# Optimization experiments

Hardware: AMD Instinct MI355X
Metric: run time of the kernel (lower is better)

The kernel has to match this reference:

```python
import jax, jax.numpy as jnp
import numpy as np

N, B, E, H = 16384, 16, 131072, 2
NPG = N // B  # nodes per graph
DIMS = [128, 256, 512]  # in==out channels per GAT layer


def setup_inputs() -> dict:
    key = jax.random.key(0)
    ks = iter(jax.random.split(key, 40))
    inp = {"node_feats": jax.random.normal(next(ks), (N, DIMS[0]), jnp.float32)}
    for l, d in enumerate(DIMS):
        s = 1.0 / np.sqrt(d)
        inp[f"W{l}"] = jax.random.normal(next(ks), (d, H * d), jnp.float32) * s
        inp[f"attnl{l}"] = jax.random.normal(next(ks), (H, d), jnp.float32) * 0.1
        inp[f"attnr{l}"] = jax.random.normal(next(ks), (H, d), jnp.float32) * 0.1
        inp[f"resW{l}"] = jax.random.normal(next(ks), (d, H * d), jnp.float32) * s
        inp[f"gamma{l}"] = jnp.ones((d,), jnp.float32)
        inp[f"beta{l}"] = jnp.zeros((d,), jnp.float32)
        inp[f"alpha{l}"] = jnp.ones((d,), jnp.float32)
    dst = jax.random.randint(next(ks), (E,), 0, N, jnp.int32)
    # source node sampled from the same graph as the destination
    src = (dst // NPG) * NPG + jax.random.randint(next(ks), (E,), 0, NPG, jnp.int32)
    inp["edge_src"] = src
    inp["edge_dst"] = dst
    inp["graph_ids"] = jnp.repeat(jnp.arange(B, dtype=jnp.int32), NPG)
    return inp


def _gat(x, W, al, ar, rW, src, dst, d):
    # x: [N, in]; W,rW: [in, H*d]; al,ar: [H,d]
    h = (x @ W).reshape(N, H, d)
    el = jnp.sum(h * al, -1)  # [N,H]
    er = jnp.sum(h * ar, -1)  # [N,H]
    e = jax.nn.leaky_relu(el[src] + er[dst], 0.2)  # [E,H]
    m = jax.ops.segment_max(e, dst, num_segments=N)
    ex = jnp.exp(e - m[dst])
    a = ex / jax.ops.segment_sum(ex, dst, num_segments=N)[dst]  # edge softmax
    out = jax.ops.segment_sum(h[src] * a[:, :, None], dst, num_segments=N)
    return out + (x @ rW).reshape(N, H, d)  # residual projection


def _gnorm(x, gamma, beta, alpha, eps=1e-5):
    # GraphNorm: (x - alpha*mean) / std * gamma + beta, stats over all nodes/heads
    mean = jnp.mean(x, axis=(0, 1), keepdims=True)
    sh = x - alpha * mean
    var = jnp.mean(sh * sh, axis=(0, 1), keepdims=True)
    return gamma * sh * jax.lax.rsqrt(var + eps) + beta


def reference(node_feats, W0, attnl0, attnr0, resW0, gamma0, beta0, alpha0,
              W1, attnl1, attnr1, resW1, gamma1, beta1, alpha1,
              W2, attnl2, attnr2, resW2, gamma2, beta2, alpha2,
              edge_src, edge_dst, graph_ids):
    params = [(W0, attnl0, attnr0, resW0, gamma0, beta0, alpha0),
              (W1, attnl1, attnr1, resW1, gamma1, beta1, alpha1),
              (W2, attnl2, attnr2, resW2, gamma2, beta2, alpha2)]
    counts = jax.ops.segment_sum(jnp.ones((N,), jnp.float32), graph_ids, num_segments=B)
    x = node_feats
    parts = []
    for l, d in enumerate(DIMS):
        W, al, ar, rW, g, b, a_ = params[l]
        x = _gat(x.reshape(N, -1), W, al, ar, rW, edge_src, edge_dst, d)  # [N,H,d]
        x = _gnorm(x, g, b, a_)
        x = jax.nn.leaky_relu(x, 0.01)
        nm = x.mean(1)  # [N,d] head-mean stored as 'updated_feats'
        parts.append(jax.ops.segment_sum(nm, graph_ids, num_segments=B) / counts[:, None])
    return jax.nn.leaky_relu(jnp.concatenate(parts, -1), 0.01)  # [B, 896]
```

## Files before the change

### kernel.cpp

```cpp
#include <hip/hip_runtime.h>
#include <math.h>

constexpr int NNODES  = 16384;
constexpr int NEDGES  = 131072;
constexpr int NGRAPHS = 16;

typedef short bf16x8 __attribute__((ext_vector_type(8)));
typedef short bf16x4 __attribute__((ext_vector_type(4)));
typedef float f32x4  __attribute__((ext_vector_type(4)));

__device__ __forceinline__ float leaky(float x, float s){ return x >= 0.0f ? x : s * x; }

__device__ __forceinline__ unsigned short f2bf(float f){
  unsigned u = __builtin_bit_cast(unsigned, f);
  u += 0x7FFFu + ((u >> 16) & 1u);
  return (unsigned short)(u >> 16);
}
__device__ __forceinline__ float bf2f(unsigned short u){
  unsigned x = (unsigned)u << 16; return __builtin_bit_cast(float, x);
}

__device__ __forceinline__ void gload_lds16(const unsigned short* g, unsigned short* l){
  __builtin_amdgcn_global_load_lds((const __attribute__((address_space(1))) void*)g,
                                   (__attribute__((address_space(3))) void*)l, 16, 0, 0);
}

__global__ void k_deg(const int* __restrict__ dst, int* __restrict__ deg){
  int e = blockIdx.x * 256 + threadIdx.x;
  if (e < NEDGES) atomicAdd(&deg[dst[e]], 1);
}

__global__ __launch_bounds__(1024) void k_scan(const int* __restrict__ deg,
                                               int* __restrict__ rowptr,
                                               int* __restrict__ cursor){
  __shared__ int sums[1024];
  int t = threadIdx.x;
  int loc[16];
  int s = 0;
  #pragma unroll
  for (int i = 0; i < 16; i++){ loc[i] = deg[t*16 + i]; s += loc[i]; }
  sums[t] = s; __syncthreads();
  for (int off = 1; off < 1024; off <<= 1){
    int v = (t >= off) ? sums[t - off] : 0;
    __syncthreads();
    sums[t] += v;
    __syncthreads();
  }
  int base = (t > 0) ? sums[t-1] : 0;
  #pragma unroll
  for (int i = 0; i < 16; i++){
    rowptr[t*16 + i] = base; cursor[t*16 + i] = base; base += loc[i];
  }
  if (t == 1023) rowptr[NNODES] = base;
}

__global__ void k_scatter(const int* __restrict__ src, const int* __restrict__ dst,
                          int* __restrict__ cursor, int* __restrict__ perm){
  int e = blockIdx.x * 256 + threadIdx.x;
  if (e < NEDGES){ int p = atomicAdd(&cursor[dst[e]], 1); perm[p] = src[e]; }
}

__global__ __launch_bounds__(256) void k_counts(const int* __restrict__ gid, float* __restrict__ counts){
  __shared__ int h[NGRAPHS];
  int t = threadIdx.x;
  if (t < NGRAPHS) h[t] = 0;
  __syncthreads();
  int base = blockIdx.x * 1024;
  #pragma unroll
  for (int i = 0; i < 4; i++)
    atomicAdd(&h[gid[base + t + i*256]], 1);
  __syncthreads();
  if (t < NGRAPHS && h[t] > 0) atomicAdd(&counts[t], (float)h[t]);
}

__global__ void k_cvt(const float* __restrict__ in, unsigned short* __restrict__ out, int n4){
  int i = blockIdx.x * 256 + threadIdx.x;
  if (i >= n4) return;
  float4 v = ((const float4*)in)[i];
  ushort4 o; o.x = f2bf(v.x); o.y = f2bf(v.y); o.z = f2bf(v.z); o.w = f2bf(v.w);
  ((ushort4*)out)[i] = o;
}

__global__ __launch_bounds__(256) void k_cvt_t2(const float* __restrict__ W,
                                                const float* __restrict__ RW,
                                                unsigned short* __restrict__ Wt,
                                                unsigned short* __restrict__ RWt,
                                                int K, int NN){
  __shared__ float tile[32][33];
  const float* src = blockIdx.z ? RW : W;
  unsigned short* dst = blockIdx.z ? RWt : Wt;
  int n0 = blockIdx.x * 32, k0 = blockIdx.y * 32;
  int tx = threadIdx.x & 31, ty = threadIdx.x >> 5;
  #pragma unroll
  for (int i = 0; i < 4; i++)
    tile[ty + i*8][tx] = src[(size_t)(k0 + ty + i*8) * NN + n0 + tx];
  __syncthreads();
  #pragma unroll
  for (int i = 0; i < 4; i++)
    dst[(size_t)(n0 + ty + i*8) * K + k0 + tx] = f2bf(tile[tx][ty + i*8]);
}

__global__ __launch_bounds__(256) void k_gemm2(const unsigned short* __restrict__ A,
                                               const unsigned short* __restrict__ Wt,
                                               const unsigned short* __restrict__ RWt,
                                               unsigned short* __restrict__ HB,
                                               unsigned short* __restrict__ RB,
                                               const float* __restrict__ al,
                                               const float* __restrict__ ar,
                                               float* __restrict__ elp,
                                               float* __restrict__ erp,
                                               int K, int NN){
  __shared__ unsigned short As[2][128 * 64];
  __shared__ unsigned short Bs[2][128 * 64];
  int t = threadIdx.x;
  int lane = t & 63, w = t >> 6;
  int nx  = gridDim.x;
  int nwg = nx * gridDim.y;
  int bid = blockIdx.x + blockIdx.y * nx;
  int wg  = (bid & 7) * (nwg >> 3) + (bid >> 3);
  int bx = wg % nx, by = wg / nx;
  int half = nx >> 1;
  bool isW = bx < half;
  const unsigned short* Bt = isW ? Wt : RWt;
  int colB = (isW ? bx : bx - half) * 128;
  int rowA = by * 128;

  int wr = (w >> 1) * 64, wc = (w & 1) * 64;
  int l16 = lane & 15, lhi = lane >> 4;
  int r8  = lane >> 3;
  int kcs = (((lane & 7) * 16) ^ (r8 << 4)) >> 1;
  f32x4 acc[4][4] = {};

  const unsigned short* Ap = A  + (size_t)(rowA) * K + kcs;
  const unsigned short* Bp = Bt + (size_t)(colB) * K + kcs;

  int nt = K >> 6;
  #pragma unroll
  for (int i = 0; i < 4; i++){
    int c = w * 4 + i;
    int row = c * 8 + r8;
    gload_lds16(Ap + (size_t)row * K, &As[0][c * 512]);
    gload_lds16(Bp + (size_t)row * K, &Bs[0][c * 512]);
  }
  __syncthreads();

  int cur = 0;
  for (int tI = 0; tI < nt; tI++){
    if (tI + 1 < nt){
      int k0n = (tI + 1) << 6;
      #pragma unroll
      for (int i = 0; i < 4; i++){
        int c = w * 4 + i;
        int row = c * 8 + r8;
        gload_lds16(Ap + (size_t)row * K + k0n, &As[cur ^ 1][c * 512]);
        gload_lds16(Bp + (size_t)row * K + k0n, &Bs[cur ^ 1][c * 512]);
      }
    }
    bf16x8 af[4][2], bfr[4][2];
    #pragma unroll
    for (int mi = 0; mi < 4; mi++){
      int row = wr + mi * 16 + l16;
      #pragma unroll
      for (int s = 0; s < 2; s++){
        int k = s * 32 + lhi * 8;
        int off = row * 128 + ((k * 2) ^ ((row & 7) << 4));
        af[mi][s] = *(const bf16x8*)((const char*)As[cur] + off);
      }
    }
    #pragma unroll
    for (int ni = 0; ni < 4; ni++){
      int row = wc + ni * 16 + l16;
      #pragma unroll
      for (int s = 0; s < 2; s++){
        int k = s * 32 + lhi * 8;
        int off = row * 128 + ((k * 2) ^ ((row & 7) << 4));
        bfr[ni][s] = *(const bf16x8*)((const char*)Bs[cur] + off);
      }
    }
    #pragma unroll
    for (int mi = 0; mi < 4; mi++)
      #pragma unroll
      for (int ni = 0; ni < 4; ni++){
        acc[mi][ni] = __builtin_amdgcn_mfma_f32_16x16x32_bf16(af[mi][0], bfr[ni][0], acc[mi][ni], 0, 0, 0);
        acc[mi][ni] = __builtin_amdgcn_mfma_f32_16x16x32_bf16(af[mi][1], bfr[ni][1], acc[mi][ni], 0, 0, 0);
      }
    __syncthreads();
    cur ^= 1;
  }

  unsigned short* C = isW ? HB : RB;
  #pragma unroll
  for (int mi = 0; mi < 4; mi++){
    #pragma unroll
    for (int j = 0; j < 4; j++){
      int r = rowA + wr + mi * 16 + lhi * 4 + j;
      unsigned short* Cp = C + (size_t)r * NN + colB + wc + l16;
      #pragma unroll
      for (int ni = 0; ni < 4; ni++)
        Cp[ni * 16] = f2bf(acc[mi][ni][j]);
    }
  }

  if (isW){
    int G = NN >> 6;
    int g64 = (colB + wc) >> 6;
    float alv[4], arv[4];
    #pragma unroll
    for (int ni = 0; ni < 4; ni++){
      int col = colB + wc + ni * 16 + l16;
      alv[ni] = al[col]; arv[ni] = ar[col];
    }
    #pragma unroll
    for (int mi = 0; mi < 4; mi++){
      #pragma unroll
      for (int j = 0; j < 4; j++){
        float pe = acc[mi][0][j]*alv[0] + acc[mi][1][j]*alv[1]
                 + acc[mi][2][j]*alv[2] + acc[mi][3][j]*alv[3];
        float pr = acc[mi][0][j]*arv[0] + acc[mi][1][j]*arv[1]
                 + acc[mi][2][j]*arv[2] + acc[mi][3][j]*arv[3];
        #pragma unroll
        for (int o = 8; o; o >>= 1){ pe += __shfl_xor(pe, o); pr += __shfl_xor(pr, o); }
        if (l16 == 0){
          int r = rowA + wr + mi * 16 + lhi * 4 + j;
          elp[(size_t)r * G + g64] = pe;
          erp[(size_t)r * G + g64] = pr;
        }
      }
    }
  }
}

__global__ void k_elred(const float* __restrict__ elp, const float* __restrict__ erp,
                        float* __restrict__ el, float* __restrict__ er, int G){
  int row = blockIdx.x * 256 + threadIdx.x;
  int half = G >> 1;
  float s0 = 0.f, s1 = 0.f, q0 = 0.f, q1 = 0.f;
  const float* ep = elp + (size_t)row * G;
  const float* rp = erp + (size_t)row * G;
  for (int i = 0; i < half; i++){ s0 += ep[i]; q0 += rp[i]; }
  for (int i = half; i < G; i++){ s1 += ep[i]; q1 += rp[i]; }
  el[row*2] = s0; el[row*2+1] = s1;
  er[row*2] = q0; er[row*2+1] = q1;
}

template<int D>
__global__ __launch_bounds__(256) void k_attn(const unsigned short* __restrict__ HB,
                                              unsigned short* __restrict__ RB,
                                              const float* __restrict__ el,
                                              const float* __restrict__ er,
                                              const int* __restrict__ rowptr,
                                              const int* __restrict__ perm){
  constexpr int ITER = (2*D)/256;
  int wid = threadIdx.x >> 6, lane = threadIdx.x & 63;
  int nb = (blockIdx.x & 7) * (NNODES/4/8) + (blockIdx.x >> 3);
  int n = nb * 4 + wid;
  int r0 = rowptr[n], r1 = rowptr[n+1];
  if (r0 == r1) return;
  float er0 = er[n*2], er1 = er[n*2+1];
  float mx0 = -1e30f, mx1 = -1e30f;
  for (int e = r0 + lane; e < r1; e += 64){
    int s = perm[e];
    mx0 = fmaxf(mx0, leaky(el[s*2]   + er0, 0.2f));
    mx1 = fmaxf(mx1, leaky(el[s*2+1] + er1, 0.2f));
  }
  #pragma unroll
  for (int o = 32; o; o >>= 1){ mx0 = fmaxf(mx0, __shfl_xor(mx0, o)); mx1 = fmaxf(mx1, __shfl_xor(mx1, o)); }
  float sm0 = 0.0f, sm1 = 0.0f;
  for (int e = r0 + lane; e < r1; e += 64){
    int s = perm[e];
    sm0 += expf(leaky(el[s*2]   + er0, 0.2f) - mx0);
    sm1 += expf(leaky(el[s*2+1] + er1, 0.2f) - mx1);
  }
  #pragma unroll
  for (int o = 32; o; o >>= 1){ sm0 += __shfl_xor(sm0, o); sm1 += __shfl_xor(sm1, o); }
  float inv0 = 1.0f / sm0, inv1 = 1.0f / sm1;
  float acc[ITER][4];
  #pragma unroll
  for (int j = 0; j < ITER; j++)
    #pragma unroll
    for (int i = 0; i < 4; i++) acc[j][i] = 0.0f;
  for (int e = r0; e < r1; ++e){
    int s = perm[e];
    float a0 = expf(leaky(el[s*2]   + er0, 0.2f) - mx0) * inv0;
    float a1 = expf(leaky(el[s*2+1] + er1, 0.2f) - mx1) * inv1;
    const unsigned short* hrow = HB + (size_t)s * (2*D);
    #pragma unroll
    for (int j = 0; j < ITER; j++){
      int base = j*256 + lane*4;
      bf16x4 v = *(const bf16x4*)(hrow + base);
      float a = (base < D) ? a0 : a1;
      #pragma unroll
      for (int i = 0; i < 4; i++)
        acc[j][i] += a * bf2f((unsigned short)v[i]);
    }
  }
  unsigned short* rrow = RB + (size_t)n * (2*D);
  #pragma unroll
  for (int j = 0; j < ITER; j++){
    int base = j*256 + lane*4;
    bf16x4 r = *(bf16x4*)(rrow + base);
    ushort4 o;
    o.x = f2bf(bf2f((unsigned short)r[0]) + acc[j][0]);
    o.y = f2bf(bf2f((unsigned short)r[1]) + acc[j][1]);
    o.z = f2bf(bf2f((unsigned short)r[2]) + acc[j][2]);
    o.w = f2bf(bf2f((unsigned short)r[3]) + acc[j][3]);
    *(ushort4*)(rrow + base) = o;
  }
}

__global__ __launch_bounds__(256) void k_stats(const unsigned short* __restrict__ R, int nn,
                                               float* __restrict__ gsum, float* __restrict__ gsq){
  int t = threadIdx.x, lane = t & 63, w = t >> 6;
  int c = blockIdx.y * 256 + lane * 4;
  const unsigned short* base = R + (size_t)(blockIdx.x * 128 + w) * nn + c;
  float4 s = make_float4(0,0,0,0), q = make_float4(0,0,0,0);
  #pragma unroll 4
  for (int i = 0; i < 32; i++){
    bf16x4 bv = *(const bf16x4*)(base + (size_t)(i * 4) * nn);
    float vx = bf2f((unsigned short)bv[0]), vy = bf2f((unsigned short)bv[1]);
    float vz = bf2f((unsigned short)bv[2]), vw = bf2f((unsigned short)bv[3]);
    s.x += vx; s.y += vy; s.z += vz; s.w += vw;
    q.x += vx*vx; q.y += vy*vy; q.z += vz*vz; q.w += vw*vw;
  }
  __shared__ float4 rs[256], rq[256];
  rs[t] = s; rq[t] = q; __syncthreads();
  if (t < 64){
    float4 a = rs[t], b = rs[t+64], c2 = rs[t+128], d2 = rs[t+192];
    float4 e = rq[t], f = rq[t+64], g2 = rq[t+128], h2 = rq[t+192];
    int cc = blockIdx.y * 256 + t * 4;
    atomicAdd(&gsum[cc+0], a.x+b.x+c2.x+d2.x);
    atomicAdd(&gsum[cc+1], a.y+b.y+c2.y+d2.y);
    atomicAdd(&gsum[cc+2], a.z+b.z+c2.z+d2.z);
    atomicAdd(&gsum[cc+3], a.w+b.w+c2.w+d2.w);
    atomicAdd(&gsq [cc+0], e.x+f.x+g2.x+h2.x);
    atomicAdd(&gsq [cc+1], e.y+f.y+g2.y+h2.y);
    atomicAdd(&gsq [cc+2], e.z+f.z+g2.z+h2.z);
    atomicAdd(&gsq [cc+3], e.w+f.w+g2.w+h2.w);
  }
}

__global__ __launch_bounds__(256) void k_norm_pool(const unsigned short* __restrict__ R,
                                                   unsigned short* __restrict__ Xn,
                                                   const float* __restrict__ gsum,
                                                   const float* __restrict__ gsq,
                                                   const float* __restrict__ gamma,
                                                   const float* __restrict__ beta,
                                                   const float* __restrict__ alpha,
                                                   float* __restrict__ pool, int d, int loff){
  int t = threadIdx.x, lane = t & 63, w = t >> 6;
  int c = blockIdx.y * 256 + lane * 4;
  int cm = c & (d - 1);
  int nodeb = blockIdx.x * 128;
  int g = blockIdx.x >> 3;
  int nn = 2 * d;
  const float Minv = 1.0f / (2.0f * (float)NNODES);
  float4 gg = *(const float4*)(gamma + cm);
  float4 bb = *(const float4*)(beta + cm);
  float4 aa = *(const float4*)(alpha + cm);
  float mmv[4], rrv[4];
  #pragma unroll
  for (int i = 0; i < 4; i++){
    float m = (gsum[cm+i] + gsum[cm+i+d]) * Minv;
    float q = (gsq [cm+i] + gsq [cm+i+d]) * Minv;
    float a = (i==0)?aa.x:(i==1)?aa.y:(i==2)?aa.z:aa.w;
    float var = q - a * m * m * (2.0f - a);
    mmv[i] = m; rrv[i] = rsqrtf(var + 1e-5f);
  }
  float am0 = aa.x*mmv[0], am1 = aa.y*mmv[1], am2 = aa.z*mmv[2], am3 = aa.w*mmv[3];
  const unsigned short* base = R + (size_t)(nodeb + w) * nn + c;
  unsigned short* xb = Xn ? (Xn + (size_t)(nodeb + w) * nn + c) : nullptr;
  float4 accp = make_float4(0,0,0,0);
  #pragma unroll 4
  for (int i = 0; i < 32; i++){
    bf16x4 bv = *(const bf16x4*)(base + (size_t)(i * 4) * nn);
    float vx = bf2f((unsigned short)bv[0]), vy = bf2f((unsigned short)bv[1]);
    float vz = bf2f((unsigned short)bv[2]), vw = bf2f((unsigned short)bv[3]);
    float y0 = gg.x*(vx-am0)*rrv[0] + bb.x; y0 = y0 >= 0.f ? y0 : 0.01f*y0;
    float y1 = gg.y*(vy-am1)*rrv[1] + bb.y; y1 = y1 >= 0.f ? y1 : 0.01f*y1;
    float y2 = gg.z*(vz-am2)*rrv[2] + bb.z; y2 = y2 >= 0.f ? y2 : 0.01f*y2;
    float y3 = gg.w*(vw-am3)*rrv[3] + bb.w; y3 = y3 >= 0.f ? y3 : 0.01f*y3;
    if (xb){
      ushort4 o; o.x = f2bf(y0); o.y = f2bf(y1); o.z = f2bf(y2); o.w = f2bf(y3);
      *(ushort4*)(xb + (size_t)(i * 4) * nn) = o;
    }
    accp.x += y0; accp.y += y1; accp.z += y2; accp.w += y3;
  }
  __shared__ float4 red[256];
  red[t] = accp; __syncthreads();
  if (t < 64){
    float4 a = red[t], b = red[t+64], c2 = red[t+128], d2 = red[t+192];
    int cc = blockIdx.y * 256 + t * 4;
    float* pb = pool + g * 896 + loff;
    atomicAdd(&pb[(cc+0) & (d-1)], 0.5f*(a.x+b.x+c2.x+d2.x));
    atomicAdd(&pb[(cc+1) & (d-1)], 0.5f*(a.y+b.y+c2.y+d2.y));
    atomicAdd(&pb[(cc+2) & (d-1)], 0.5f*(a.z+b.z+c2.z+d2.z));
    atomicAdd(&pb[(cc+3) & (d-1)], 0.5f*(a.w+b.w+c2.w+d2.w));
  }
}

__global__ void k_final(const float* __restrict__ pool, const float* __restrict__ counts,
                        float* __restrict__ out){
  int idx = blockIdx.x * 256 + threadIdx.x;
  if (idx >= NGRAPHS * 896) return;
  int g = idx / 896;
  float v = pool[idx] / counts[g];
  out[idx] = v >= 0.0f ? v : 0.01f * v;
}

extern "C" void kernel_launch(void* const* d_in, const int* in_sizes, int n_in,
                              void* d_out, int out_size, void* d_ws, size_t ws_size,
                              hipStream_t stream){
  const float* x0 = (const float*)d_in[0];
  const float *W[3], *AL[3], *AR[3], *RW[3], *GA[3], *BE[3], *ALP[3];
  for (int l = 0; l < 3; l++){
    const int b = 1 + l*7;
    W[l]  = (const float*)d_in[b+0];
    AL[l] = (const float*)d_in[b+1];
    AR[l] = (const float*)d_in[b+2];
    RW[l] = (const float*)d_in[b+3];
    GA[l] = (const float*)d_in[b+4];
    BE[l] = (const float*)d_in[b+5];
    ALP[l]= (const float*)d_in[b+6];
  }
  const int* esrc = (const int*)d_in[22];
  const int* edst = (const int*)d_in[23];
  const int* gid  = (const int*)d_in[24];
  float* out = (float*)d_out;

  char* p = (char*)d_ws;
  auto carve = [&](size_t bytes)->void*{
    void* r = (void*)p; p += (bytes + 255) & ~(size_t)255; return r;
  };
  unsigned short* HB = (unsigned short*)carve((size_t)NNODES * 1024 * 2);
  unsigned short* RB = (unsigned short*)carve((size_t)NNODES * 1024 * 2);
  unsigned short* X0b = (unsigned short*)carve((size_t)NNODES * 128 * 2);
  unsigned short* XA  = (unsigned short*)carve((size_t)NNODES * 256 * 2);
  unsigned short* XB  = (unsigned short*)carve((size_t)NNODES * 512 * 2);
  unsigned short* Wt  = (unsigned short*)carve((size_t)1024 * 512 * 2);
  unsigned short* RWt = (unsigned short*)carve((size_t)1024 * 512 * 2);
  float* el     = (float*)carve((size_t)NNODES * 2 * 4);
  float* er     = (float*)carve((size_t)NNODES * 2 * 4);
  float* elp    = (float*)carve((size_t)NNODES * 16 * 4);
  float* erp    = (float*)carve((size_t)NNODES * 16 * 4);
  int*   deg    = (int*)  carve((size_t)NNODES * 4);
  int*   rowptr = (int*)  carve((size_t)(NNODES + 1) * 4);
  int*   cursor = (int*)  carve((size_t)NNODES * 4);
  int*   perm   = (int*)  carve((size_t)NEDGES * 4);
  float* stats  = (float*)carve(2048 * 4);
  float* pool   = (float*)carve((size_t)NGRAPHS * 896 * 4);
  float* countsF= (float*)carve((size_t)NGRAPHS * 4);
  (void)ws_size; (void)in_sizes; (void)n_in; (void)out_size;

  hipMemsetAsync(deg, 0, NNODES * 4, stream);
  hipMemsetAsync(pool, 0, NGRAPHS * 896 * 4, stream);
  hipMemsetAsync(countsF, 0, NGRAPHS * 4, stream);

  k_deg    <<<NEDGES/256, 256, 0, stream>>>(edst, deg);
  k_scan   <<<1, 1024, 0, stream>>>(deg, rowptr, cursor);
  k_scatter<<<NEDGES/256, 256, 0, stream>>>(esrc, edst, cursor, perm);
  k_counts <<<NNODES/1024, 256, 0, stream>>>(gid, countsF);
  k_cvt    <<<(NNODES*128/4 + 255)/256, 256, 0, stream>>>(x0, X0b, NNODES*128/4);

  const unsigned short* xin = X0b;
  int loff = 0;
  const int dims[3] = {128, 256, 512};
  for (int l = 0; l < 3; l++){
    int d = dims[l], nn = 2*d;
    dim3 gt(nn/32, d/32, 2);
    k_cvt_t2<<<gt, 256, 0, stream>>>(W[l], RW[l], Wt, RWt, d, nn);
    dim3 gg(2*nn/128, NNODES/128);
    k_gemm2<<<gg, 256, 0, stream>>>(xin, Wt, RWt, HB, RB, AL[l], AR[l], elp, erp, d, nn);
    k_elred<<<NNODES/256, 256, 0, stream>>>(elp, erp, el, er, nn >> 6);
    if (d == 128){
      k_attn<128><<<NNODES/4, 256, 0, stream>>>(HB, RB, el, er, rowptr, perm);
    } else if (d == 256){
      k_attn<256><<<NNODES/4, 256, 0, stream>>>(HB, RB, el, er, rowptr, perm);
    } else {
      k_attn<512><<<NNODES/4, 256, 0, stream>>>(HB, RB, el, er, rowptr, perm);
    }
    hipMemsetAsync(stats, 0, 2048 * 4, stream);
    dim3 gs(NNODES/128, nn/256);
    k_stats   <<<gs, 256, 0, stream>>>(RB, nn, stats, stats + 1024);
    unsigned short* xn = (l == 0) ? XA : (l == 1) ? XB : nullptr;
    k_norm_pool<<<gs, 256, 0, stream>>>(RB, xn, stats, stats + 1024, GA[l], BE[l], ALP[l], pool, d, loff);
    xin = xn; loff += d;
  }
  k_final<<<(NGRAPHS*896 + 255)/256, 256, 0, stream>>>(pool, countsF, out);
}
```

Before: 341.6 us.

## Compute W and residual projections together sharing the A tile, drop double buffering

Each GEMM workgroup now computes a 128x64 tile of both the attention projection and the residual projection, loading the shared A tile once and reusing it for two B tiles instead of splitting W and RW across separate workgroups. Double buffering of LDS is removed in favour of a single-buffer load/sync/compute loop, and el/er partials are produced at 32-column granularity across all workgroups. This halves A-tile global traffic but loses the prefetch overlap and makes each warp's tile narrower, which may expose load latency.

```diff
diff --git a/kernel.cpp b/kernel.cpp
--- a/kernel.cpp
+++ b/kernel.cpp
@@ -110,8 +110,9 @@
                                                float* __restrict__ elp,
                                                float* __restrict__ erp,
                                                int K, int NN){
-  __shared__ unsigned short As[2][128 * 64];
-  __shared__ unsigned short Bs[2][128 * 64];
+  __shared__ unsigned short As[128 * 64];
+  __shared__ unsigned short Ws[64 * 64];
+  __shared__ unsigned short Rs[64 * 64];
   int t = threadIdx.x;
   int lane = t & 63, w = t >> 6;
   int nx  = gridDim.x;
@@ -119,111 +120,95 @@
   int bid = blockIdx.x + blockIdx.y * nx;
   int wg  = (bid & 7) * (nwg >> 3) + (bid >> 3);
   int bx = wg % nx, by = wg / nx;
-  int half = nx >> 1;
-  bool isW = bx < half;
-  const unsigned short* Bt = isW ? Wt : RWt;
-  int colB = (isW ? bx : bx - half) * 128;
+  int colB = bx * 64;
   int rowA = by * 128;
 
-  int wr = (w >> 1) * 64, wc = (w & 1) * 64;
+  int wr = (w >> 1) * 64, wc = (w & 1) * 32;
   int l16 = lane & 15, lhi = lane >> 4;
   int r8  = lane >> 3;
   int kcs = (((lane & 7) * 16) ^ (r8 << 4)) >> 1;
-  f32x4 acc[4][4] = {};
-
-  const unsigned short* Ap = A  + (size_t)(rowA) * K + kcs;
-  const unsigned short* Bp = Bt + (size_t)(colB) * K + kcs;
-
-  int nt = K >> 6;
-  #pragma unroll
-  for (int i = 0; i < 4; i++){
-    int c = w * 4 + i;
-    int row = c * 8 + r8;
-    gload_lds16(Ap + (size_t)row * K, &As[0][c * 512]);
-    gload_lds16(Bp + (size_t)row * K, &Bs[0][c * 512]);
-  }
-  __syncthreads();
-
-  int cur = 0;
-  for (int tI = 0; tI < nt; tI++){
-    if (tI + 1 < nt){
-      int k0n = (tI + 1) << 6;
-      #pragma unroll
-      for (int i = 0; i < 4; i++){
-        int c = w * 4 + i;
-        int row = c * 8 + r8;
-        gload_lds16(Ap + (size_t)row * K + k0n, &As[cur ^ 1][c * 512]);
-        gload_lds16(Bp + (size_t)row * K + k0n, &Bs[cur ^ 1][c * 512]);
+
+  f32x4 accW[4][2] = {};
+  f32x4 accR[4][2] = {};
+
+  const unsigned short* Ap = A   + (size_t)rowA * K + kcs;
+  const unsigned short* Wp = Wt  + (size_t)colB * K + kcs;
+  const unsigned short* Rp = RWt + (size_t)colB * K + kcs;
+
+  for (int k0 = 0; k0 < K; k0 += 64){
+    __syncthreads();
+    #pragma unroll
+    for (int i = 0; i < 4; i++){
+      int c = w * 4 + i;
+      gload_lds16(Ap + (size_t)(c * 8 + r8) * K + k0, &As[c * 512]);
+    }
+    #pragma unroll
+    for (int i = 0; i < 2; i++){
+      int c = w * 2 + i;
+      size_t go = (size_t)(c * 8 + r8) * K + k0;
+      gload_lds16(Wp + go, &Ws[c * 512]);
+      gload_lds16(Rp + go, &Rs[c * 512]);
+    }
+    __syncthreads();
+    #pragma unroll
+    for (int s = 0; s < 2; s++){
+      int k = s * 32 + lhi * 8;
+      bf16x8 af[4], bw[2], br[2];
+      #pragma unroll
+      for (int mi = 0; mi < 4; mi++){
+        int row = wr + mi * 16 + l16;
+        int off = row * 128 + ((k * 2) ^ ((row & 7) << 4));
+        af[mi] = *(const bf16x8*)((const char*)As + off);
       }
-    }
-    bf16x8 af[4][2], bfr[4][2];
-    #pragma unroll
-    for (int mi = 0; mi < 4; mi++){
-      int row = wr + mi * 16 + l16;
-      #pragma unroll
-      for (int s = 0; s < 2; s++){
-        int k = s * 32 + lhi * 8;
+      #pragma unroll
+      for (int ni = 0; ni < 2; ni++){
+        int row = wc + ni * 16 + l16;
         int off = row * 128 + ((k * 2) ^ ((row & 7) << 4));
-        af[mi][s] = *(const bf16x8*)((const char*)As[cur] + off);
+        bw[ni] = *(const bf16x8*)((const char*)Ws + off);
+        br[ni] = *(const bf16x8*)((const char*)Rs + off);
       }
-    }
-    #pragma unroll
-    for (int ni = 0; ni < 4; ni++){
-      int row = wc + ni * 16 + l16;
-      #pragma unroll
-      for (int s = 0; s < 2; s++){
-        int k = s * 32 + lhi * 8;
-        int off = row * 128 + ((k * 2) ^ ((row & 7) << 4));
-        bfr[ni][s] = *(const bf16x8*)((const char*)Bs[cur] + off);
-      }
-    }
-    #pragma unroll
-    for (int mi = 0; mi < 4; mi++)
-      #pragma unroll
-      for (int ni = 0; ni < 4; ni++){
-        acc[mi][ni] = __builtin_amdgcn_mfma_f32_16x16x32_bf16(af[mi][0], bfr[ni][0], acc[mi][ni], 0, 0, 0);
-        acc[mi][ni] = __builtin_amdgcn_mfma_f32_16x16x32_bf16(af[mi][1], bfr[ni][1], acc[mi][ni], 0, 0, 0);
-      }
-    __syncthreads();
-    cur ^= 1;
-  }
-
-  unsigned short* C = isW ? HB : RB;
+      #pragma unroll
+      for (int mi = 0; mi < 4; mi++)
+        #pragma unroll
+        for (int ni = 0; ni < 2; ni++){
+          accW[mi][ni] = __builtin_amdgcn_mfma_f32_16x16x32_bf16(af[mi], bw[ni], accW[mi][ni], 0, 0, 0);
+          accR[mi][ni] = __builtin_amdgcn_mfma_f32_16x16x32_bf16(af[mi], br[ni], accR[mi][ni], 0, 0, 0);
+        }
+    }
+  }
+
   #pragma unroll
   for (int mi = 0; mi < 4; mi++){
     #pragma unroll
     for (int j = 0; j < 4; j++){
       int r = rowA + wr + mi * 16 + lhi * 4 + j;
-      unsigned short* Cp = C + (size_t)r * NN + colB + wc + l16;
-      #pragma unroll
-      for (int ni = 0; ni < 4; ni++)
-        Cp[ni * 16] = f2bf(acc[mi][ni][j]);
-    }
-  }
-
-  if (isW){
-    int G = NN >> 6;
-    int g64 = (colB + wc) >> 6;
-    float alv[4], arv[4];
-    #pragma unroll
-    for (int ni = 0; ni < 4; ni++){
-      int col = colB + wc + ni * 16 + l16;
-      alv[ni] = al[col]; arv[ni] = ar[col];
-    }
+      unsigned short* Hp  = HB + (size_t)r * NN + colB + wc + l16;
+      unsigned short* Rp2 = RB + (size_t)r * NN + colB + wc + l16;
+      #pragma unroll
+      for (int ni = 0; ni < 2; ni++){
+        Hp[ni * 16]  = f2bf(accW[mi][ni][j]);
+        Rp2[ni * 16] = f2bf(accR[mi][ni][j]);
+      }
+    }
+  }
+
+  {
+    int G = NN >> 5;
+    int g32 = (colB + wc) >> 5;
+    float alv0 = al[colB + wc + l16],      arv0 = ar[colB + wc + l16];
+    float alv1 = al[colB + wc + 16 + l16], arv1 = ar[colB + wc + 16 + l16];
     #pragma unroll
     for (int mi = 0; mi < 4; mi++){
       #pragma unroll
       for (int j = 0; j < 4; j++){
-        float pe = acc[mi][0][j]*alv[0] + acc[mi][1][j]*alv[1]
-                 + acc[mi][2][j]*alv[2] + acc[mi][3][j]*alv[3];
-        float pr = acc[mi][0][j]*arv[0] + acc[mi][1][j]*arv[1]
-                 + acc[mi][2][j]*arv[2] + acc[mi][3][j]*arv[3];
+        float pe = accW[mi][0][j]*alv0 + accW[mi][1][j]*alv1;
+        float pr = accW[mi][0][j]*arv0 + accW[mi][1][j]*arv1;
         #pragma unroll
         for (int o = 8; o; o >>= 1){ pe += __shfl_xor(pe, o); pr += __shfl_xor(pr, o); }
         if (l16 == 0){
           int r = rowA + wr + mi * 16 + lhi * 4 + j;
-          elp[(size_t)r * G + g64] = pe;
-          erp[(size_t)r * G + g64] = pr;
+          elp[(size_t)r * G + g32] = pe;
+          erp[(size_t)r * G + g32] = pr;
         }
       }
     }
@@ -440,8 +425,8 @@
   unsigned short* RWt = (unsigned short*)carve((size_t)1024 * 512 * 2);
   float* el     = (float*)carve((size_t)NNODES * 2 * 4);
   float* er     = (float*)carve((size_t)NNODES * 2 * 4);
-  float* elp    = (float*)carve((size_t)NNODES * 16 * 4);
-  float* erp    = (float*)carve((size_t)NNODES * 16 * 4);
+  float* elp    = (float*)carve((size_t)NNODES * 32 * 4);
+  float* erp    = (float*)carve((size_t)NNODES * 32 * 4);
   int*   deg    = (int*)  carve((size_t)NNODES * 4);
   int*   rowptr = (int*)  carve((size_t)(NNODES + 1) * 4);
   int*   cursor = (int*)  carve((size_t)NNODES * 4);
@@ -468,9 +453,9 @@
     int d = dims[l], nn = 2*d;
     dim3 gt(nn/32, d/32, 2);
     k_cvt_t2<<<gt, 256, 0, stream>>>(W[l], RW[l], Wt, RWt, d, nn);
-    dim3 gg(2*nn/128, NNODES/128);
+    dim3 gg(nn/64, NNODES/128);
     k_gemm2<<<gg, 256, 0, stream>>>(xin, Wt, RWt, HB, RB, AL[l], AR[l], elp, erp, d, nn);
-    k_elred<<<NNODES/256, 256, 0, stream>>>(elp, erp, el, er, nn >> 6);
+    k_elred<<<NNODES/256, 256, 0, stream>>>(elp, erp, el, er, nn >> 5);
     if (d == 128){
       k_attn<128><<<NNODES/4, 256, 0, stream>>>(HB, RB, el, er, rowptr, perm);
     } else if (d == 256){
```

New measurement: 343.0 us. No clear change (+0.4%).
